# Kernel optimization log

Measured on AMD Instinct MI355X. Metric: run time of the kernel, lower is better.

Reference implementation:

```python
import jax, jax.numpy as jnp
import numpy as np

B, T, D, H = 32, 2048, 256, 256

def setup_inputs() -> dict:
    key = jax.random.key(0)
    k1, k2, k3 = jax.random.split(key, 3)
    s_x = 1.0 / np.sqrt(D)
    s_h = 1.0 / np.sqrt(H)
    return {
        "x": jax.random.normal(k1, (B, T, D), dtype=jnp.float32),
        "W_x": jax.random.normal(k2, (D, 3 * H), dtype=jnp.float32) * s_x,
        "W_h": jax.random.normal(k3, (H, 3 * H), dtype=jnp.float32) * s_h,
        "b": jnp.zeros((3 * H,), dtype=jnp.float32),
    }

def reference(x, W_x, W_h, b):
    # GRU cell unrolled over time; state starts at zeros (reset_state=True).
    # Precompute input projections for all timesteps in one big GEMM: [B,T,3H]
    x_proj = jnp.einsum("btd,dg->btg", x, W_x) + b
    h0 = jnp.zeros((x.shape[0], H), dtype=x.dtype)

    def step(h, xp_t):
        xz, xr, xn = jnp.split(xp_t, 3, axis=-1)          # each [B,H]
        hz, hr, hn = jnp.split(h @ W_h, 3, axis=-1)        # each [B,H]
        z = jax.nn.sigmoid(xz + hz)
        r = jax.nn.sigmoid(xr + hr)
        n = jnp.tanh(xn + r * hn)
        h_new = z * h + (1.0 - z) * n
        return h_new, h_new

    # scan over time (axis 1 -> move to leading axis)
    _, ys = jax.lax.scan(step, h0, jnp.swapaxes(x_proj, 0, 1))
    return jnp.swapaxes(ys, 0, 1)  # [B,T,H]
```

## Files before the change

kernel.cpp:

```cpp
#include <hip/hip_runtime.h>

#define Bb 32
#define Tt 2048
#define Dd 256
#define Hh 256
#define G3 768

typedef _Float16 f16x8 __attribute__((ext_vector_type(8)));
typedef float f32x4 __attribute__((ext_vector_type(4)));
union H2U { unsigned u; _Float16 h[2]; };
union V16 { uint4 u; f16x8 f; };

__device__ __forceinline__ float frcpf(float x) {
#if __has_builtin(__builtin_amdgcn_rcpf)
    return __builtin_amdgcn_rcpf(x);
#else
    return 1.0f / x;
#endif
}
__device__ __forceinline__ float sigmoidf_(float s) { return frcpf(1.0f + __expf(-s)); }
__device__ __forceinline__ float tanhf_(float u) {
    float e = __expf(2.0f * u);
    return 1.0f - 2.0f * frcpf(e + 1.0f);
}

__global__ void cvt_x_kernel(const float* __restrict__ x, _Float16* __restrict__ xo) {
    const size_t i = ((size_t)blockIdx.x * 256 + threadIdx.x) * 4;
    float4 v = *reinterpret_cast<const float4*>(x + i);
    H2U a, b;
    a.h[0] = (_Float16)v.x; a.h[1] = (_Float16)v.y;
    b.h[0] = (_Float16)v.z; b.h[1] = (_Float16)v.w;
    uint2 o; o.x = a.u; o.y = b.u;
    *reinterpret_cast<uint2*>(xo + i) = o;
}

__global__ void wxt_kernel(const float* __restrict__ Wx, _Float16* __restrict__ wxt) {
    const int o = blockIdx.x * 256 + threadIdx.x;
    const int n = o >> 7, kp = o & 127;
    float f0 = Wx[(size_t)(2 * kp) * G3 + n];
    float f1 = Wx[(size_t)(2 * kp + 1) * G3 + n];
    H2U u; u.h[0] = (_Float16)f0; u.h[1] = (_Float16)f1;
    reinterpret_cast<unsigned*>(wxt)[o] = u.u;
}

__global__ __launch_bounds__(256)
void gemm_xp_kernel(const _Float16* __restrict__ A, const _Float16* __restrict__ Bm,
                    const float* __restrict__ bias, _Float16* __restrict__ xp) {
    __shared__ _Float16 As[128][264];
    __shared__ _Float16 Bs[64][264];
    const int tid = threadIdx.x;
    const int m0 = (blockIdx.x / 12) * 128;
    const int n0 = (blockIdx.x % 12) * 64;

#pragma unroll
    for (int it = 0; it < 16; ++it) {
        int c = tid + it * 256, row = c >> 5, col = c & 31;
        uint4 v = *reinterpret_cast<const uint4*>(A + (size_t)(m0 + row) * 256 + col * 8);
        *reinterpret_cast<uint4*>(&As[row][col * 8]) = v;
    }
#pragma unroll
    for (int it = 0; it < 8; ++it) {
        int c = tid + it * 256, row = c >> 5, col = c & 31;
        uint4 v = *reinterpret_cast<const uint4*>(Bm + (size_t)(n0 + row) * 256 + col * 8);
        *reinterpret_cast<uint4*>(&Bs[row][col * 8]) = v;
    }
    __syncthreads();

    const int wave = tid >> 6, lane = tid & 63;
    const int wr = wave >> 1, wc = wave & 1;
    const int r16 = lane & 15, kg = lane >> 4;

    f32x4 acc[4][2];
#pragma unroll
    for (int mi = 0; mi < 4; ++mi)
#pragma unroll
        for (int ni = 0; ni < 2; ++ni) acc[mi][ni] = (f32x4){0.f, 0.f, 0.f, 0.f};

    float bv[2];
#pragma unroll
    for (int ni = 0; ni < 2; ++ni) bv[ni] = bias[n0 + wc * 32 + ni * 16 + r16];

#pragma unroll
    for (int kk = 0; kk < 8; ++kk) {
        f16x8 a[4], b2[2];
#pragma unroll
        for (int mi = 0; mi < 4; ++mi) {
            V16 t; t.u = *reinterpret_cast<const uint4*>(&As[wr * 64 + mi * 16 + r16][kk * 32 + kg * 8]);
            a[mi] = t.f;
        }
#pragma unroll
        for (int ni = 0; ni < 2; ++ni) {
            V16 t; t.u = *reinterpret_cast<const uint4*>(&Bs[wc * 32 + ni * 16 + r16][kk * 32 + kg * 8]);
            b2[ni] = t.f;
        }
#pragma unroll
        for (int mi = 0; mi < 4; ++mi)
#pragma unroll
            for (int ni = 0; ni < 2; ++ni)
                acc[mi][ni] = __builtin_amdgcn_mfma_f32_16x16x32_f16(a[mi], b2[ni], acc[mi][ni], 0, 0, 0);
    }

#pragma unroll
    for (int mi = 0; mi < 4; ++mi)
#pragma unroll
        for (int ni = 0; ni < 2; ++ni)
#pragma unroll
            for (int r = 0; r < 4; ++r) {
                int row = m0 + wr * 64 + mi * 16 + kg * 4 + r;
                int col = n0 + wc * 32 + ni * 16 + r16;
                xp[(size_t)row * G3 + col] = (_Float16)(acc[mi][ni][r] + bv[ni]);
            }
}

#define GSTEP(PR, PW, T)                                                              \
  {                                                                                   \
                    \
    const _Float16* xnp = xq + (size_t)((T) + 1 < Tt ? (T) + 1 : (T)) * G3;           \
    _Float16 pz = xnp[0], pr = xnp[Hh], pn = xnp[2 * Hh];                             \
                \
    f16x8 af[8];                                                                      \
    _Pragma("unroll") for (int ks = 0; ks < 8; ++ks) {                                \
      V16 t;                                                                          \
      t.u = *reinterpret_cast<const uint4*>(                                          \
          reinterpret_cast<const char*>(&hs[PR][0]) + ks * 64 + kg * 16);             \
      af[ks] = t.f;                                                                   \
    }                                                                                 \
                                            \
    f16x8 sb[3][2][2];                                                                \
    _Pragma("unroll") for (int g = 0; g < 3; ++g)                                     \
      _Pragma("unroll") for (int sub = 0; sub < 2; ++sub)                             \
        _Pragma("unroll") for (int ksl = 0; ksl < 2; ++ksl) {                         \
          const int n = g * Hh + C0 + sub * 16 + col16;                               \
          V16 t;                                                                      \
          t.u = *reinterpret_cast<const uint4*>(                                      \
              reinterpret_cast<const char*>(wlds) + (ksl * 768 + n) * 80 + kg * 16);  \
          sb[g][sub][ksl] = t.f;                                                      \
        }                                                                             \
    f32x4 acc[3][2];                                                                  \
    _Pragma("unroll") for (int g = 0; g < 3; ++g)                                     \
      _Pragma("unroll") for (int sub = 0; sub < 2; ++sub)                             \
        acc[g][sub] = (f32x4){0.f, 0.f, 0.f, 0.f};                                    \
    _Pragma("unroll") for (int ks = 0; ks < 6; ++ks)                                  \
      _Pragma("unroll") for (int g = 0; g < 3; ++g)                                   \
        _Pragma("unroll") for (int sub = 0; sub < 2; ++sub)                           \
          acc[g][sub] = __builtin_amdgcn_mfma_f32_16x16x32_f16(                       \
              af[ks], bfr[g][sub][ks], acc[g][sub], 0, 0, 0);                         \
    _Pragma("unroll") for (int ksl = 0; ksl < 2; ++ksl)                               \
      _Pragma("unroll") for (int g = 0; g < 3; ++g)                                   \
        _Pragma("unroll") for (int sub = 0; sub < 2; ++sub)                           \
          acc[g][sub] = __builtin_amdgcn_mfma_f32_16x16x32_f16(                       \
              af[6 + ksl], sb[g][sub][ksl], acc[g][sub], 0, 0, 0);                    \
                         \
    float hz = sel ? acc[0][1][0] : acc[0][0][0];                                     \
    float hr = sel ? acc[1][1][0] : acc[1][0][0];                                     \
    float hn = sel ? acc[2][1][0] : acc[2][0][0];                                     \
    float zg = sigmoidf_(xz + hz);                                                    \
    float rg = sigmoidf_(xr + hr);                                                    \
    float ng = tanhf_(xn + rg * hn);                                                  \
    float hnew = zg * hprev + (1.0f - zg) * ng;                                       \
    hprev = hnew;                                                                     \
    if (lane < 32) {                                                                  \
      hs[PW][C0 + lcol] = (_Float16)hnew;                                             \
      yb[(size_t)(T) * Hh] = hnew;                                                    \
    }                                                                                 \
    xz = (float)pz; xr = (float)pr; xn = (float)pn;                                   \
    __builtin_amdgcn_sched_barrier(0);                                                \
    asm volatile("s_waitcnt lgkmcnt(0)" ::: "memory");                                \
    __builtin_amdgcn_s_barrier();                                                     \
    __builtin_amdgcn_sched_barrier(0);                                                \
  }

__global__ __launch_bounds__(512, 2)
void gru_scan_kernel(const _Float16* __restrict__ xp, const float* __restrict__ Wh,
                     float* __restrict__ y) {
    __shared__ __align__(16) _Float16 wlds[2 * 768 * 40];
    __shared__ __align__(16) _Float16 hs[2][256];

    const int tid = threadIdx.x;
    const int b = blockIdx.x;
    const int wave = tid >> 6, lane = tid & 63;
    const int col16 = lane & 15, kg = lane >> 4;
    const int sel = (lane >> 4) & 1;
    const int lcol = lane & 31;
    const int C0 = 32 * wave;

    f16x8 bfr[3][2][6];
#pragma unroll
    for (int g = 0; g < 3; ++g)
#pragma unroll
        for (int sub = 0; sub < 2; ++sub)
#pragma unroll
            for (int ks = 0; ks < 6; ++ks) {
                V16 t;
#pragma unroll
                for (int j = 0; j < 8; ++j) {
                    const int k = 32 * ks + 8 * kg + j;
                    t.f[j] = (_Float16)Wh[(size_t)k * G3 + g * Hh + C0 + sub * 16 + col16];
                }
                bfr[g][sub][ks] = t.f;
            }

    for (int kp = 0; kp < 32; ++kp) {
        const int k = 192 + 2 * kp;
        const int ksl = (k >> 5) - 6;
        const int koff = k & 31;
        for (int n = tid; n < 768; n += 512) {
            float f0 = Wh[(size_t)k * G3 + n];
            float f1 = Wh[(size_t)(k + 1) * G3 + n];
            H2U u; u.h[0] = (_Float16)f0; u.h[1] = (_Float16)f1;
            *reinterpret_cast<unsigned*>(
                reinterpret_cast<char*>(wlds) + (ksl * 768 + n) * 80 + koff * 2) = u.u;
        }
    }

    if (tid < 256) { hs[0][tid] = (_Float16)0.f; hs[1][tid] = (_Float16)0.f; }

    const _Float16* xq = xp + (size_t)b * Tt * G3 + C0 + lcol;
    float* yb = y + (size_t)b * Tt * Hh + C0 + lcol;
    float xz = (float)xq[0], xr = (float)xq[Hh], xn = (float)xq[2 * Hh];
    float hprev = 0.0f;

    __syncthreads();

#pragma unroll 1
    for (int t = 0; t < Tt; t += 2) {
        GSTEP(0, 1, t);
        GSTEP(1, 0, t + 1);
    }
}

extern "C" void kernel_launch(void* const* d_in, const int* in_sizes, int n_in,
                              void* d_out, int out_size, void* d_ws, size_t ws_size,
                              hipStream_t stream) {
    (void)in_sizes; (void)n_in; (void)out_size; (void)ws_size;
    const float* x    = (const float*)d_in[0];
    const float* Wx   = (const float*)d_in[1];
    const float* Wh   = (const float*)d_in[2];
    const float* bias = (const float*)d_in[3];
    float* y = (float*)d_out;

    _Float16* xp   = (_Float16*)d_ws;
    _Float16* xf16 = (_Float16*)d_out;
    _Float16* wxt  = (_Float16*)((char*)d_out + (size_t)33554432);

    cvt_x_kernel<<<dim3(16384), dim3(256), 0, stream>>>(x, xf16);
    wxt_kernel<<<dim3(384), dim3(256), 0, stream>>>(Wx, wxt);
    gemm_xp_kernel<<<dim3(6144), dim3(256), 0, stream>>>(xf16, wxt, bias, xp);
    gru_scan_kernel<<<dim3(Bb), dim3(512), 0, stream>>>(xp, Wh, y);
}
```

Measured before the change: 2.201 ms.

## Replace per-step MFMA recurrence with register-resident fdot2 matvec and DPP reductions

Each thread now holds a 64-element K-slice of W_h for two output columns across all three gates in registers (192 packed half2 values). The per-step h@W_h is computed with v_dot2 instructions and reduced across the 4 K-splitting lanes with DPP xor shuffles. This replaces the MFMA-based matvec, which wasted most of the 16-row tile on a single batch row and read part of W_h from LDS every step. The 192 weight registers per thread under launch_bounds(512,2) risk spilling, and the per-step matvec now runs on scalar VALU dot-product instructions instead of matrix cores.

```diff
diff --git a/kernel.cpp b/kernel.cpp
--- a/kernel.cpp
+++ b/kernel.cpp
@@ -6,10 +6,21 @@
 #define Hh 256
 #define G3 768
 
+typedef _Float16 h2_t __attribute__((ext_vector_type(2)));
 typedef _Float16 f16x8 __attribute__((ext_vector_type(8)));
 typedef float f32x4 __attribute__((ext_vector_type(4)));
-union H2U { unsigned u; _Float16 h[2]; };
+union H2U { unsigned u; _Float16 h[2]; h2_t v; };
 union V16 { uint4 u; f16x8 f; };
+
+__device__ __forceinline__ float fdot2f(unsigned a, unsigned b, float c) {
+#if __has_builtin(__builtin_amdgcn_fdot2)
+    H2U ua, ub; ua.u = a; ub.u = b;
+    return __builtin_amdgcn_fdot2(ua.v, ub.v, c, false);
+#else
+    H2U ua, ub; ua.u = a; ub.u = b;
+    return c + (float)ua.h[0] * (float)ub.h[0] + (float)ua.h[1] * (float)ub.h[1];
+#endif
+}
 
 __device__ __forceinline__ float frcpf(float x) {
 #if __has_builtin(__builtin_amdgcn_rcpf)
@@ -22,6 +33,12 @@
 __device__ __forceinline__ float tanhf_(float u) {
     float e = __expf(2.0f * u);
     return 1.0f - 2.0f * frcpf(e + 1.0f);
+}
+__device__ __forceinline__ float dpp_xor1(float v) {
+    return __int_as_float(__builtin_amdgcn_update_dpp(0, __float_as_int(v), 0xB1, 0xF, 0xF, true));
+}
+__device__ __forceinline__ float dpp_xor2(float v) {
+    return __int_as_float(__builtin_amdgcn_update_dpp(0, __float_as_int(v), 0x4E, 0xF, 0xF, true));
 }
 
 __global__ void cvt_x_kernel(const float* __restrict__ x, _Float16* __restrict__ xo) {
@@ -112,56 +129,61 @@
             }
 }
 
+#define GDOT(HF)                                                                      \
+  {                                                                                   \
+    uint4 h0 = hq[(HF) * 2 + 0];                                                      \
+    uint4 h1 = hq[(HF) * 2 + 1];                                                      \
+    _Pragma("unroll") for (int u = 0; u < 4; ++u) {                                   \
+      const unsigned hu = (u == 0) ? h0.x : (u == 1) ? h0.y : (u == 2) ? h0.z : h0.w; \
+      sz0 = fdot2f(w[0][0][(HF) * 8 + u], hu, sz0);                                   \
+      sr0 = fdot2f(w[1][0][(HF) * 8 + u], hu, sr0);                                   \
+      sn0 = fdot2f(w[2][0][(HF) * 8 + u], hu, sn0);                                   \
+      sz1 = fdot2f(w[0][1][(HF) * 8 + u], hu, sz1);                                   \
+      sr1 = fdot2f(w[1][1][(HF) * 8 + u], hu, sr1);                                   \
+      sn1 = fdot2f(w[2][1][(HF) * 8 + u], hu, sn1);                                   \
+    }                                                                                 \
+    _Pragma("unroll") for (int u = 0; u < 4; ++u) {                                   \
+      const unsigned hu = (u == 0) ? h1.x : (u == 1) ? h1.y : (u == 2) ? h1.z : h1.w; \
+      sz0 = fdot2f(w[0][0][(HF) * 8 + 4 + u], hu, sz0);                               \
+      sr0 = fdot2f(w[1][0][(HF) * 8 + 4 + u], hu, sr0);                               \
+      sn0 = fdot2f(w[2][0][(HF) * 8 + 4 + u], hu, sn0);                               \
+      sz1 = fdot2f(w[0][1][(HF) * 8 + 4 + u], hu, sz1);                               \
+      sr1 = fdot2f(w[1][1][(HF) * 8 + 4 + u], hu, sr1);                               \
+      sn1 = fdot2f(w[2][1][(HF) * 8 + 4 + u], hu, sn1);                               \
+    }                                                                                 \
+  }
+
 #define GSTEP(PR, PW, T)                                                              \
   {                                                                                   \
-                    \
+              \
+                   \
     const _Float16* xnp = xq + (size_t)((T) + 1 < Tt ? (T) + 1 : (T)) * G3;           \
     _Float16 pz = xnp[0], pr = xnp[Hh], pn = xnp[2 * Hh];                             \
-                \
-    f16x8 af[8];                                                                      \
-    _Pragma("unroll") for (int ks = 0; ks < 8; ++ks) {                                \
-      V16 t;                                                                          \
-      t.u = *reinterpret_cast<const uint4*>(                                          \
-          reinterpret_cast<const char*>(&hs[PR][0]) + ks * 64 + kg * 16);             \
-      af[ks] = t.f;                                                                   \
-    }                                                                                 \
-                                            \
-    f16x8 sb[3][2][2];                                                                \
-    _Pragma("unroll") for (int g = 0; g < 3; ++g)                                     \
-      _Pragma("unroll") for (int sub = 0; sub < 2; ++sub)                             \
-        _Pragma("unroll") for (int ksl = 0; ksl < 2; ++ksl) {                         \
-          const int n = g * Hh + C0 + sub * 16 + col16;                               \
-          V16 t;                                                                      \
-          t.u = *reinterpret_cast<const uint4*>(                                      \
-              reinterpret_cast<const char*>(wlds) + (ksl * 768 + n) * 80 + kg * 16);  \
-          sb[g][sub][ksl] = t.f;                                                      \
-        }                                                                             \
-    f32x4 acc[3][2];                                                                  \
-    _Pragma("unroll") for (int g = 0; g < 3; ++g)                                     \
-      _Pragma("unroll") for (int sub = 0; sub < 2; ++sub)                             \
-        acc[g][sub] = (f32x4){0.f, 0.f, 0.f, 0.f};                                    \
-    _Pragma("unroll") for (int ks = 0; ks < 6; ++ks)                                  \
-      _Pragma("unroll") for (int g = 0; g < 3; ++g)                                   \
-        _Pragma("unroll") for (int sub = 0; sub < 2; ++sub)                           \
-          acc[g][sub] = __builtin_amdgcn_mfma_f32_16x16x32_f16(                       \
-              af[ks], bfr[g][sub][ks], acc[g][sub], 0, 0, 0);                         \
-    _Pragma("unroll") for (int ksl = 0; ksl < 2; ++ksl)                               \
-      _Pragma("unroll") for (int g = 0; g < 3; ++g)                                   \
-        _Pragma("unroll") for (int sub = 0; sub < 2; ++sub)                           \
-          acc[g][sub] = __builtin_amdgcn_mfma_f32_16x16x32_f16(                       \
-              af[6 + ksl], sb[g][sub][ksl], acc[g][sub], 0, 0, 0);                    \
-                         \
-    float hz = sel ? acc[0][1][0] : acc[0][0][0];                                     \
-    float hr = sel ? acc[1][1][0] : acc[1][0][0];                                     \
-    float hn = sel ? acc[2][1][0] : acc[2][0][0];                                     \
-    float zg = sigmoidf_(xz + hz);                                                    \
-    float rg = sigmoidf_(xr + hr);                                                    \
-    float ng = tanhf_(xn + rg * hn);                                                  \
-    float hnew = zg * hprev + (1.0f - zg) * ng;                                       \
+    float sz0 = 0.f, sz1 = 0.f, sr0 = 0.f, sr1 = 0.f, sn0 = 0.f, sn1 = 0.f;           \
+    const uint4* hq = reinterpret_cast<const uint4*>(&hbuf[PR][q * 36]);              \
+    GDOT(0) GDOT(1) GDOT(2) GDOT(3)                                                   \
+                                \
+    sz0 += dpp_xor1(sz0); sz1 += dpp_xor1(sz1);                                       \
+    sr0 += dpp_xor1(sr0); sr1 += dpp_xor1(sr1);                                       \
+    sn0 += dpp_xor1(sn0); sn1 += dpp_xor1(sn1);                                       \
+    sz0 += dpp_xor2(sz0); sz1 += dpp_xor2(sz1);                                       \
+    sr0 += dpp_xor2(sr0); sr1 += dpp_xor2(sr1);                                       \
+    sn0 += dpp_xor2(sn0); sn1 += dpp_xor2(sn1);                                       \
+    const float hz = (q & 1) ? sz1 : sz0;                                             \
+    const float hr = (q & 1) ? sr1 : sr0;                                             \
+    const float hn = (q & 1) ? sn1 : sn0;                                             \
+    const float zg = sigmoidf_(xz + hz);                                              \
+    const float rg = sigmoidf_(xr + hr);                                              \
+    const float ng = tanhf_(xn + rg * hn);                                            \
+    const float hnew = zg * hprev + (1.0f - zg) * ng;                                 \
     hprev = hnew;                                                                     \
-    if (lane < 32) {                                                                  \
-      hs[PW][C0 + lcol] = (_Float16)hnew;                                             \
-      yb[(size_t)(T) * Hh] = hnew;                                                    \
+    H2U hc; hc.h[0] = (_Float16)hnew; hc.h[1] = (_Float16)0.f;                        \
+    const unsigned pu = (unsigned)__builtin_amdgcn_update_dpp(0, (int)hc.u, 0xB1, 0xF, 0xF, true); \
+    const int pf = __builtin_amdgcn_update_dpp(0, __float_as_int(hnew), 0xB1, 0xF, 0xF, true);      \
+    if (q == 0) {                                                                     \
+      hbuf[PW][(slot >> 5) * 36 + (slot & 31)] = (hc.u & 0xFFFFu) | (pu << 16);       \
+      float2 yv; yv.x = hnew; yv.y = __int_as_float(pf);                              \
+      *reinterpret_cast<float2*>(yb + (size_t)(T) * Hh) = yv;                         \
     }                                                                                 \
     xz = (float)pz; xr = (float)pr; xn = (float)pn;                                   \
     __builtin_amdgcn_sched_barrier(0);                                                \
@@ -173,52 +195,37 @@
 __global__ __launch_bounds__(512, 2)
 void gru_scan_kernel(const _Float16* __restrict__ xp, const float* __restrict__ Wh,
                      float* __restrict__ y) {
-    __shared__ __align__(16) _Float16 wlds[2 * 768 * 40];
-    __shared__ __align__(16) _Float16 hs[2][256];
+    __shared__ unsigned hbuf[2][144];
 
     const int tid = threadIdx.x;
     const int b = blockIdx.x;
-    const int wave = tid >> 6, lane = tid & 63;
-    const int col16 = lane & 15, kg = lane >> 4;
-    const int sel = (lane >> 4) & 1;
-    const int lcol = lane & 31;
-    const int C0 = 32 * wave;
-
-    f16x8 bfr[3][2][6];
-#pragma unroll
-    for (int g = 0; g < 3; ++g)
-#pragma unroll
-        for (int sub = 0; sub < 2; ++sub)
-#pragma unroll
-            for (int ks = 0; ks < 6; ++ks) {
-                V16 t;
-#pragma unroll
-                for (int j = 0; j < 8; ++j) {
-                    const int k = 32 * ks + 8 * kg + j;
-                    t.f[j] = (_Float16)Wh[(size_t)k * G3 + g * Hh + C0 + sub * 16 + col16];
-                }
-                bfr[g][sub][ks] = t.f;
-            }
-
-    for (int kp = 0; kp < 32; ++kp) {
-        const int k = 192 + 2 * kp;
-        const int ksl = (k >> 5) - 6;
-        const int koff = k & 31;
-        for (int n = tid; n < 768; n += 512) {
-            float f0 = Wh[(size_t)k * G3 + n];
-            float f1 = Wh[(size_t)(k + 1) * G3 + n];
-            H2U u; u.h[0] = (_Float16)f0; u.h[1] = (_Float16)f1;
-            *reinterpret_cast<unsigned*>(
-                reinterpret_cast<char*>(wlds) + (ksl * 768 + n) * 80 + koff * 2) = u.u;
+    const int q = tid & 3;
+    const int slot = tid >> 2;
+
+    unsigned w[3][2][32];
+#pragma unroll
+    for (int g = 0; g < 3; ++g) {
+        const int c0 = g * Hh + 2 * slot;
+#pragma unroll
+        for (int kp = 0; kp < 32; ++kp) {
+            const int k = 64 * q + 2 * kp;
+            float2 f0 = *reinterpret_cast<const float2*>(Wh + (size_t)k * G3 + c0);
+            float2 f1 = *reinterpret_cast<const float2*>(Wh + (size_t)(k + 1) * G3 + c0);
+            H2U p0, p1;
+            p0.h[0] = (_Float16)f0.x; p0.h[1] = (_Float16)f1.x;
+            p1.h[0] = (_Float16)f0.y; p1.h[1] = (_Float16)f1.y;
+            w[g][0][kp] = p0.u;
+            w[g][1][kp] = p1.u;
         }
     }
 
-    if (tid < 256) { hs[0][tid] = (_Float16)0.f; hs[1][tid] = (_Float16)0.f; }
-
-    const _Float16* xq = xp + (size_t)b * Tt * G3 + C0 + lcol;
-    float* yb = y + (size_t)b * Tt * Hh + C0 + lcol;
+    if (tid < 288) hbuf[tid / 144][tid % 144] = 0u;
+    float hprev = 0.0f;
+
+    const int j = 2 * slot + (q & 1);
+    const _Float16* xq = xp + (size_t)b * Tt * G3 + j;
+    float* yb = y + (size_t)b * Tt * Hh + 2 * slot;
     float xz = (float)xq[0], xr = (float)xq[Hh], xn = (float)xq[2 * Hh];
-    float hprev = 0.0f;
 
     __syncthreads();
 
```

Result: no change. 2.190 ms (-0.5%).
